# Kernel tuning notes

Measured on AMD Instinct MI355X. Metric: run time of the kernel, lower is better.

The kernel has to match this reference:

```python
import jax, jax.numpy as jnp
import numpy as np

B, S, D, E = 4, 4096, 1024, 8

def setup_inputs() -> dict:
    key = jax.random.key(0)
    k1, k2, k3, k4, k5 = jax.random.split(key, 5)
    scale = 1.0 / np.sqrt(D)
    return {
        "x": jax.random.normal(k1, (B, S, D), dtype=jnp.float32),
        "Wg": jax.random.normal(k2, (D, D), dtype=jnp.float32) * scale,   # gate Linear(D, D)
        "bg": jnp.zeros((D,), dtype=jnp.float32),
        "We": jax.random.normal(k3, (E, D, D), dtype=jnp.float32) * scale,  # per-expert Linear(D, D)
        "be": jnp.zeros((E, D), dtype=jnp.float32),
    }

def reference(x, Wg, bg, We, be):
    # gating network: Linear + Softmax over last dim (size D, per the original module)
    probs = jax.nn.softmax(x @ Wg + bg, axis=-1)           # [B,S,D]
    idx = jnp.argmax(probs, axis=-1)                        # [B,S], values in [0, D)
    p = jnp.take_along_axis(probs, idx[..., None], axis=-1)[..., 0]  # top-1 gate prob
    e_idx = idx % We.shape[0]                               # map argmax to expert id
    # run every expert densely, then select routed expert per token (top-1 switch routing)
    h = jax.nn.relu(jnp.einsum('bsd,edf->besf', x, We) + be[None, :, None, :])  # [B,E,S,D]
    onehot = jax.nn.one_hot(e_idx, We.shape[0], dtype=x.dtype)                   # [B,S,E]
    out = jnp.einsum('besf,bse->bsf', h, onehot) * p[..., None]                  # [B,S,D]
    return out
```

## Files before the change

kernel.cpp:

```cpp
#include <hip/hip_runtime.h>
#include <stdint.h>
#include <stddef.h>

#define TOK    16384
#define DDIM   1024
#define NEXP   8
#define BMT    128
#define RB_MAX 136
#define MARGIN 2.5e-2f
#define AMBIG_CAP 4096
#define BK     64

typedef __bf16 bf16x8 __attribute__((ext_vector_type(8)));
typedef float  f32x4  __attribute__((ext_vector_type(4)));
typedef unsigned short u16x8 __attribute__((ext_vector_type(8)));

__device__ __forceinline__ unsigned short f2bf(float f) {
    unsigned int u = __float_as_uint(f);
    u += 0x7fff + ((u >> 16) & 1);
    return (unsigned short)(u >> 16);
}

__device__ __forceinline__ void gload_lds16(const void* g, void* l) {
    __builtin_amdgcn_global_load_lds(
        (const __attribute__((address_space(1))) unsigned int*)g,
        (__attribute__((address_space(3))) unsigned int*)l, 16, 0, 0);
}

__device__ __forceinline__ void seg_starts(const int* __restrict__ cnt, int* st) {
    int total = 0;
#pragma unroll
    for (int e = 0; e < NEXP; e++) {
        st[e] = total;
        total += ((cnt[e] + BMT - 1) / BMT) * BMT;
    }
    st[NEXP] = total;
}

__global__ __launch_bounds__(256) void cvt_x_init(
    const float* __restrict__ x, unsigned short* __restrict__ xbf,
    int* __restrict__ cnt, int* __restrict__ cursor,
    int* __restrict__ n_ambig, int* __restrict__ row_of_slot)
{
    if (blockIdx.x == 0) {
        for (int i = threadIdx.x; i < RB_MAX * BMT; i += 256) row_of_slot[i] = -1;
        if (threadIdx.x < NEXP) { cnt[threadIdx.x] = 0; cursor[threadIdx.x] = 0; }
        if (threadIdx.x == 0) *n_ambig = 0;
    }
    const size_t t = ((size_t)blockIdx.x * 256 + threadIdx.x) * 8;
    const float4 v0 = *(const float4*)(x + t);
    const float4 v1 = *(const float4*)(x + t + 4);
    const float vv[8] = {v0.x, v0.y, v0.z, v0.w, v1.x, v1.y, v1.z, v1.w};
    u16x8 hh;
#pragma unroll
    for (int j = 0; j < 8; j++) hh[j] = f2bf(vv[j]);
    *(u16x8*)(xbf + t) = hh;
}

__global__ __launch_bounds__(256) void transpose_mat(
    const float* __restrict__ src0, unsigned short* __restrict__ dst0)
{
    __shared__ float tile[32][33];
    const int e  = blockIdx.z;
    const int k0 = blockIdx.x * 32;
    const int n0 = blockIdx.y * 32;
    const int tx = threadIdx.x;
    const int ty = threadIdx.y;
    const float* src = src0 + (size_t)e * DDIM * DDIM;
    unsigned short* dst = dst0 + (size_t)e * DDIM * DDIM;
#pragma unroll
    for (int r = 0; r < 4; r++)
        tile[ty + r * 8][tx] = src[(size_t)(k0 + ty + r * 8) * DDIM + n0 + tx];
    __syncthreads();
#pragma unroll
    for (int r = 0; r < 4; r++)
        dst[(size_t)(n0 + ty + r * 8) * DDIM + k0 + tx] = f2bf(tile[tx][ty + r * 8]);
}

__global__ __launch_bounds__(256) void transpose_wg(
    const float* __restrict__ src, unsigned short* __restrict__ dstb,
    float* __restrict__ dstf)
{
    __shared__ float tile[32][33];
    const int k0 = blockIdx.x * 32;
    const int n0 = blockIdx.y * 32;
    const int tx = threadIdx.x;
    const int ty = threadIdx.y;
#pragma unroll
    for (int r = 0; r < 4; r++)
        tile[ty + r * 8][tx] = src[(size_t)(k0 + ty + r * 8) * DDIM + n0 + tx];
    __syncthreads();
#pragma unroll
    for (int r = 0; r < 4; r++) {
        const float v = tile[tx][ty + r * 8];
        const size_t o = (size_t)(n0 + ty + r * 8) * DDIM + k0 + tx;
        dstb[o] = f2bf(v);
        dstf[o] = v;
    }
}

__global__ __launch_bounds__(256) void gating_mfma(
    const unsigned short* __restrict__ xbf,
    const unsigned short* __restrict__ WgT,
    const float* __restrict__ bg, float* __restrict__ logits)
{
    __shared__ unsigned short Asm[128 * BK];
    __shared__ unsigned short Bsm[128 * BK];
    const int bid = blockIdx.x;
    const int xcd = bid & 7;
    const int seq = bid >> 3;
    const int cl  = seq >> 6;
    const int w   = seq & 63;
    const int rb  = xcd * 16 + (w >> 2);
    const int nb  = cl * 4 + (w & 3);
    const int tid  = threadIdx.x;
    const int lane = tid & 63;
    const int wave = tid >> 6;
    const int q    = lane >> 4;
    const int m16  = lane & 15;
    const int wrow = (wave & 1) * 64;
    const int wcol = (wave >> 1) * 64;

    const unsigned short* Ag = xbf + (size_t)rb * 128 * DDIM;
    const unsigned short* Bg = WgT + (size_t)nb * 128 * DDIM;

    const unsigned short* pa[4];
    const unsigned short* pb[4];
#pragma unroll
    for (int i = 0; i < 4; i++) {
        const int idx = tid + i * 256;
        const int r = idx >> 3;
        const int c = idx & 7;
        const int g = (c ^ (r & 7)) * 8;
        pa[i] = Ag + (size_t)r * DDIM + g;
        pb[i] = Bg + (size_t)r * DDIM + g;
    }

    f32x4 acc[4][4];
#pragma unroll
    for (int i = 0; i < 4; i++)
#pragma unroll
        for (int j = 0; j < 4; j++) acc[i][j] = (f32x4){0.f, 0.f, 0.f, 0.f};

    for (int k0 = 0; k0 < DDIM; k0 += BK) {
#pragma unroll
        for (int i = 0; i < 4; i++) {
            gload_lds16(pa[i] + k0, &Asm[(tid + i * 256) * 8]);
            gload_lds16(pb[i] + k0, &Bsm[(tid + i * 256) * 8]);
        }
        __syncthreads();
#pragma unroll
        for (int s = 0; s < 2; s++) {
            const int cs = (((s << 2) + q) ^ (m16 & 7)) << 3;
            bf16x8 af[4], bfr[4];
#pragma unroll
            for (int i = 0; i < 4; i++)
                af[i] = *(const bf16x8*)&Asm[(wrow + i * 16 + m16) * BK + cs];
#pragma unroll
            for (int j = 0; j < 4; j++)
                bfr[j] = *(const bf16x8*)&Bsm[(wcol + j * 16 + m16) * BK + cs];
#pragma unroll
            for (int i = 0; i < 4; i++)
#pragma unroll
                for (int j = 0; j < 4; j++)
                    acc[i][j] = __builtin_amdgcn_mfma_f32_16x16x32_bf16(
                        af[i], bfr[j], acc[i][j], 0, 0, 0);
        }
        __syncthreads();
    }

    float bgv[4];
#pragma unroll
    for (int j = 0; j < 4; j++) bgv[j] = bg[nb * 128 + wcol + j * 16 + m16];
#pragma unroll
    for (int i = 0; i < 4; i++)
#pragma unroll
        for (int r = 0; r < 4; r++) {
            const int row = rb * 128 + wrow + i * 16 + q * 4 + r;
#pragma unroll
            for (int j = 0; j < 4; j++) {
                const int col = nb * 128 + wcol + j * 16 + m16;
                logits[(size_t)row * DDIM + col] = acc[i][j][r] + bgv[j];
            }
        }
}

__global__ __launch_bounds__(256) void row_stats(
    const float* __restrict__ logits, float* __restrict__ pout,
    int* __restrict__ eout, float* __restrict__ rmax_a, float* __restrict__ s_a,
    int* __restrict__ ambig, int* __restrict__ n_ambig)
{
    const int row  = blockIdx.x * 4 + (threadIdx.x >> 6);
    const int lane = threadIdx.x & 63;
    const float* L = logits + (size_t)row * DDIM;
    float vals[16];
#pragma unroll
    for (int i = 0; i < 4; i++)
        *(float4*)&vals[i * 4] = *(const float4*)&L[lane * 16 + i * 4];
    float m = vals[0]; int mi = lane * 16;
#pragma unroll
    for (int i = 1; i < 16; i++)
        if (vals[i] > m) { m = vals[i]; mi = lane * 16 + i; }
    for (int off = 32; off > 0; off >>= 1) {
        float ov = __shfl_down(m, off, 64);
        int   oi = __shfl_down(mi, off, 64);
        if (ov > m || (ov == m && oi < mi)) { m = ov; mi = oi; }
    }
    m  = __shfl(m, 0, 64);
    mi = __shfl(mi, 0, 64);
    float s = 0.f;
    int   c = 0;
#pragma unroll
    for (int i = 0; i < 16; i++) {
        s += expf(vals[i] - m);
        if (vals[i] >= m - MARGIN) c++;
    }
    for (int off = 32; off > 0; off >>= 1) {
        s += __shfl_xor(s, off, 64);
        c += __shfl_xor(c, off, 64);
    }
    if (lane == 0) {
        pout[row] = 1.0f / s;
        eout[row] = mi & (NEXP - 1);
        rmax_a[row] = m;
        s_a[row] = s;
        if (c > 1) {
            int k = atomicAdd(n_ambig, 1);
            if (k < AMBIG_CAP) ambig[k] = row;
        }
    }
}

__global__ __launch_bounds__(64) void fixup(
    const float* __restrict__ logits, const float* __restrict__ x,
    const float* __restrict__ WgTf, const float* __restrict__ bg,
    const float* __restrict__ rmax_a, const float* __restrict__ s_a,
    const int* __restrict__ ambig, const int* __restrict__ n_ambig,
    int* __restrict__ eout, float* __restrict__ pout)
{
    int n = *n_ambig; if (n > AMBIG_CAP) n = AMBIG_CAP;
    if ((int)blockIdx.x >= n) return;
    const int row  = ambig[blockIdx.x];
    const int lane = threadIdx.x;
    const float rmax = rmax_a[row];
    const float* L = logits + (size_t)row * DDIM;
    __shared__ int scnt;
    __shared__ int scol[32];
    if (lane == 0) scnt = 0;
    __syncthreads();
    for (int j = lane; j < DDIM; j += 64)
        if (L[j] >= rmax - MARGIN) {
            int k = atomicAdd(&scnt, 1);
            if (k < 32) scol[k] = j;
        }
    __syncthreads();
    int ncand = scnt < 32 ? scnt : 32;
    double bestv = -1e300; int bestc = DDIM;
    for (int cidx = 0; cidx < ncand; cidx++) {
        const int col = scol[cidx];
        const float* Wcol = WgTf + (size_t)col * DDIM;
        double s = 0.0;
        for (int k = lane; k < DDIM; k += 64)
            s += (double)x[(size_t)row * DDIM + k] * (double)Wcol[k];
        for (int off = 32; off > 0; off >>= 1) s += __shfl_down(s, off, 64);
        s = __shfl(s, 0, 64);
        s += (double)bg[col];
        if (s > bestv || (s == bestv && col < bestc)) { bestv = s; bestc = col; }
    }
    if (lane == 0) {
        eout[row] = bestc & (NEXP - 1);
        pout[row] = expf(L[bestc] - rmax) / s_a[row];
    }
}

__global__ __launch_bounds__(256) void histo(const int* __restrict__ eout,
                                             int* __restrict__ cnt)
{
    __shared__ int h[NEXP];
    if (threadIdx.x < NEXP) h[threadIdx.x] = 0;
    __syncthreads();
    const int t = blockIdx.x * 256 + threadIdx.x;
    if (t < TOK) atomicAdd(&h[eout[t]], 1);
    __syncthreads();
    if (threadIdx.x < NEXP) atomicAdd(&cnt[threadIdx.x], h[threadIdx.x]);
}

__global__ __launch_bounds__(256) void assign_slots(
    const int* __restrict__ eout, const int* __restrict__ cnt,
    int* __restrict__ cursor, int* __restrict__ row_of_slot)
{
    __shared__ int h[NEXP];
    __shared__ int base[NEXP];
    __shared__ int sstart[NEXP];
    const int tid = threadIdx.x;
    if (tid < NEXP) {
        h[tid] = 0;
        int st[NEXP + 1];
        seg_starts(cnt, st);
        sstart[tid] = st[tid];
    }
    __syncthreads();
    const int t = blockIdx.x * 256 + tid;
    int e = 0, lr = 0;
    if (t < TOK) {
        e = eout[t];
        lr = atomicAdd(&h[e], 1);
    }
    __syncthreads();
    if (tid < NEXP && h[tid] > 0)
        base[tid] = atomicAdd(&cursor[tid], h[tid]);
    __syncthreads();
    if (t < TOK)
        row_of_slot[sstart[e] + base[e] + lr] = t;
}

__global__ __launch_bounds__(256) void expert_gemm(
    const unsigned short* __restrict__ xbf, const unsigned short* __restrict__ WeT,
    const float* __restrict__ be, const float* __restrict__ p,
    const int* __restrict__ row_of_slot, const int* __restrict__ cnt,
    float* __restrict__ out)
{
    __shared__ unsigned short Asm[128 * BK];
    __shared__ unsigned short Bsm[128 * BK];
    __shared__ int rs[128];
    const int bid = blockIdx.x;
    const int xcd = bid & 7;
    const int seq = bid >> 3;
    const int cl  = seq / 68;
    const int w   = seq % 68;
    const int rb  = xcd * 17 + (w >> 2);
    const int nb  = cl * 4 + (w & 3);

    int st[NEXP + 1];
    seg_starts(cnt, st);
    const int s0 = rb * BMT;
    int e = -1;
#pragma unroll
    for (int ei = 0; ei < NEXP; ei++)
        if (s0 >= st[ei] && s0 < st[ei + 1]) e = ei;
    if (e < 0) return;

    const int tid  = threadIdx.x;
    const int lane = tid & 63;
    const int wave = tid >> 6;
    const int q    = lane >> 4;
    const int m16  = lane & 15;
    const int wrow = (wave & 1) * 64;
    const int wcol = (wave >> 1) * 64;

    if (tid < 128) rs[tid] = row_of_slot[rb * 128 + tid];
    __syncthreads();

    const unsigned short* Bglob = WeT + (size_t)e * DDIM * DDIM + (size_t)nb * 128 * DDIM;

    const unsigned short* pa[4];
    const unsigned short* pb[4];
#pragma unroll
    for (int i = 0; i < 4; i++) {
        const int idx = tid + i * 256;
        const int r = idx >> 3;
        const int c = idx & 7;
        const int g = (c ^ (r & 7)) * 8;
        int tr = rs[r]; if (tr < 0) tr = 0;
        pa[i] = xbf + (size_t)tr * DDIM + g;
        pb[i] = Bglob + (size_t)r * DDIM + g;
    }

    f32x4 acc[4][4];
#pragma unroll
    for (int i = 0; i < 4; i++)
#pragma unroll
        for (int j = 0; j < 4; j++) acc[i][j] = (f32x4){0.f, 0.f, 0.f, 0.f};

    for (int k0 = 0; k0 < DDIM; k0 += BK) {
#pragma unroll
        for (int i = 0; i < 4; i++) {
            gload_lds16(pa[i] + k0, &Asm[(tid + i * 256) * 8]);
            gload_lds16(pb[i] + k0, &Bsm[(tid + i * 256) * 8]);
        }
        __syncthreads();
#pragma unroll
        for (int s = 0; s < 2; s++) {
            const int cs = (((s << 2) + q) ^ (m16 & 7)) << 3;
            bf16x8 af[4], bfr[4];
#pragma unroll
            for (int i = 0; i < 4; i++)
                af[i] = *(const bf16x8*)&Asm[(wrow + i * 16 + m16) * BK + cs];
#pragma unroll
            for (int j = 0; j < 4; j++)
                bfr[j] = *(const bf16x8*)&Bsm[(wcol + j * 16 + m16) * BK + cs];
#pragma unroll
            for (int i = 0; i < 4; i++)
#pragma unroll
                for (int j = 0; j < 4; j++)
                    acc[i][j] = __builtin_amdgcn_mfma_f32_16x16x32_bf16(
                        af[i], bfr[j], acc[i][j], 0, 0, 0);
        }
        __syncthreads();
    }

    float bev[4];
#pragma unroll
    for (int j = 0; j < 4; j++) bev[j] = be[e * DDIM + nb * 128 + wcol + j * 16 + m16];
#pragma unroll
    for (int i = 0; i < 4; i++)
#pragma unroll
        for (int r = 0; r < 4; r++) {
            const int t = rs[wrow + i * 16 + q * 4 + r];
            if (t < 0) continue;
            const float pv = p[t];
#pragma unroll
            for (int j = 0; j < 4; j++) {
                const int n = nb * 128 + wcol + j * 16 + m16;
                float v = acc[i][j][r] + bev[j];
                v = v > 0.f ? v : 0.f;
                out[(size_t)t * DDIM + n] = v * pv;
            }
        }
}

extern "C" void kernel_launch(void* const* d_in, const int* in_sizes, int n_in,
                              void* d_out, int out_size, void* d_ws, size_t ws_size,
                              hipStream_t stream)
{
    const float* x  = (const float*)d_in[0];
    const float* Wg = (const float*)d_in[1];
    const float* bg = (const float*)d_in[2];
    const float* We = (const float*)d_in[3];
    const float* be = (const float*)d_in[4];
    float* out = (float*)d_out;

    char* ws = (char*)d_ws;
    float* logits = (float*)ws;                 ws += (size_t)TOK * DDIM * 4;
    unsigned short* WeT = (unsigned short*)ws;  ws += (size_t)NEXP * DDIM * DDIM * 2;
    unsigned short* WgT = (unsigned short*)ws;  ws += (size_t)DDIM * DDIM * 2;
    float* WgTf = (float*)ws;                   ws += (size_t)DDIM * DDIM * 4;
    unsigned short* xbf = (unsigned short*)ws;  ws += (size_t)TOK * DDIM * 2;
    float* p = (float*)ws;                      ws += (size_t)TOK * 4;
    int* e_arr = (int*)ws;                      ws += (size_t)TOK * 4;
    float* rmax_a = (float*)ws;                 ws += (size_t)TOK * 4;
    float* s_a = (float*)ws;                    ws += (size_t)TOK * 4;
    int* row_of_slot = (int*)ws;                ws += (size_t)RB_MAX * BMT * 4;
    int* cnt = (int*)ws;                        ws += NEXP * 4;
    int* cursor = (int*)ws;                     ws += NEXP * 4;
    int* ambig = (int*)ws;                      ws += AMBIG_CAP * 4;
    int* n_ambig = (int*)ws;                    ws += 4;

    cvt_x_init<<<TOK * DDIM / (256 * 8), 256, 0, stream>>>(
        x, xbf, cnt, cursor, n_ambig, row_of_slot);
    transpose_wg<<<dim3(32, 32), dim3(32, 8), 0, stream>>>(Wg, WgT, WgTf);
    transpose_mat<<<dim3(32, 32, NEXP), dim3(32, 8), 0, stream>>>(We, WeT);
    gating_mfma<<<1024, 256, 0, stream>>>(xbf, WgT, bg, logits);
    row_stats<<<TOK / 4, 256, 0, stream>>>(logits, p, e_arr, rmax_a, s_a, ambig, n_ambig);
    fixup<<<AMBIG_CAP, 64, 0, stream>>>(logits, x, WgTf, bg, rmax_a, s_a, ambig, n_ambig, e_arr, p);
    histo<<<TOK / 256, 256, 0, stream>>>(e_arr, cnt);
    assign_slots<<<TOK / 256, 256, 0, stream>>>(e_arr, cnt, cursor, row_of_slot);
    expert_gemm<<<1088, 256, 0, stream>>>(
        xbf, WeT, be, p, row_of_slot, cnt, out);
}
```

Baseline: 310.8 us.

## Fuse per-row softmax partial stats into gating GEMM epilogue and merge histogram

The gating GEMM epilogue now computes, for each row and each 64-column slice, the partial max, argmax, exp-sum and near-max count, and writes them to a small partials buffer. A new row_combine kernel merges the 16 partials per row instead of rereading the full 64 MB logits matrix. The same kernel also builds the expert histogram, which removes the separate histo launch. fixup now corrects the counts with atomics when it changes a token's expert. This adds shuffles and a 4 MB partials write to the GEMM epilogue, and the ambiguity count across slices is approximated by counting a non-winning slice within the margin as two candidates.

After: 317.5 us. +2.2%, slower.

```diff
diff --git a/kernel.cpp b/kernel.cpp
--- a/kernel.cpp
+++ b/kernel.cpp
@@ -102,7 +102,8 @@
 __global__ __launch_bounds__(256) void gating_mfma(
     const unsigned short* __restrict__ xbf,
     const unsigned short* __restrict__ WgT,
-    const float* __restrict__ bg, float* __restrict__ logits)
+    const float* __restrict__ bg, float* __restrict__ logits,
+    float4* __restrict__ part)
 {
     __shared__ unsigned short Asm[128 * BK];
     __shared__ unsigned short Bsm[128 * BK];
@@ -172,63 +173,85 @@
     float bgv[4];
 #pragma unroll
     for (int j = 0; j < 4; j++) bgv[j] = bg[nb * 128 + wcol + j * 16 + m16];
+    const int nbh = nb * 2 + (wave >> 1);
 #pragma unroll
     for (int i = 0; i < 4; i++)
 #pragma unroll
         for (int r = 0; r < 4; r++) {
             const int row = rb * 128 + wrow + i * 16 + q * 4 + r;
+            float v[4];
+            float vmax = -1e30f; int vidx = 0;
 #pragma unroll
             for (int j = 0; j < 4; j++) {
+                v[j] = acc[i][j][r] + bgv[j];
                 const int col = nb * 128 + wcol + j * 16 + m16;
-                logits[(size_t)row * DDIM + col] = acc[i][j][r] + bgv[j];
-            }
-        }
-}
-
-__global__ __launch_bounds__(256) void row_stats(
-    const float* __restrict__ logits, float* __restrict__ pout,
+                logits[(size_t)row * DDIM + col] = v[j];
+                if (v[j] > vmax) { vmax = v[j]; vidx = col; }
+            }
+#pragma unroll
+            for (int off = 8; off > 0; off >>= 1) {
+                float ov = __shfl_xor(vmax, off, 64);
+                int   oi = __shfl_xor(vidx, off, 64);
+                if (ov > vmax || (ov == vmax && oi < vidx)) { vmax = ov; vidx = oi; }
+            }
+            float sg = 0.f; int cg = 0;
+#pragma unroll
+            for (int j = 0; j < 4; j++) {
+                sg += expf(v[j] - vmax);
+                cg += (v[j] >= vmax - MARGIN) ? 1 : 0;
+            }
+#pragma unroll
+            for (int off = 8; off > 0; off >>= 1) {
+                sg += __shfl_xor(sg, off, 64);
+                cg += __shfl_xor(cg, off, 64);
+            }
+            if (m16 == 0) {
+                float4 pr;
+                pr.x = vmax; pr.y = __int_as_float(vidx);
+                pr.z = sg;   pr.w = __int_as_float(cg);
+                part[(size_t)row * 16 + nbh] = pr;
+            }
+        }
+}
+
+__global__ __launch_bounds__(256) void row_combine(
+    const float4* __restrict__ part, float* __restrict__ pout,
     int* __restrict__ eout, float* __restrict__ rmax_a, float* __restrict__ s_a,
-    int* __restrict__ ambig, int* __restrict__ n_ambig)
-{
-    const int row  = blockIdx.x * 4 + (threadIdx.x >> 6);
-    const int lane = threadIdx.x & 63;
-    const float* L = logits + (size_t)row * DDIM;
-    float vals[16];
-#pragma unroll
-    for (int i = 0; i < 4; i++)
-        *(float4*)&vals[i * 4] = *(const float4*)&L[lane * 16 + i * 4];
-    float m = vals[0]; int mi = lane * 16;
-#pragma unroll
-    for (int i = 1; i < 16; i++)
-        if (vals[i] > m) { m = vals[i]; mi = lane * 16 + i; }
-    for (int off = 32; off > 0; off >>= 1) {
-        float ov = __shfl_down(m, off, 64);
-        int   oi = __shfl_down(mi, off, 64);
-        if (ov > m || (ov == m && oi < mi)) { m = ov; mi = oi; }
-    }
-    m  = __shfl(m, 0, 64);
-    mi = __shfl(mi, 0, 64);
-    float s = 0.f;
-    int   c = 0;
-#pragma unroll
-    for (int i = 0; i < 16; i++) {
-        s += expf(vals[i] - m);
-        if (vals[i] >= m - MARGIN) c++;
-    }
-    for (int off = 32; off > 0; off >>= 1) {
-        s += __shfl_xor(s, off, 64);
-        c += __shfl_xor(c, off, 64);
-    }
-    if (lane == 0) {
-        pout[row] = 1.0f / s;
-        eout[row] = mi & (NEXP - 1);
-        rmax_a[row] = m;
-        s_a[row] = s;
-        if (c > 1) {
-            int k = atomicAdd(n_ambig, 1);
-            if (k < AMBIG_CAP) ambig[k] = row;
-        }
-    }
+    int* __restrict__ ambig, int* __restrict__ n_ambig, int* __restrict__ cnt)
+{
+    __shared__ int h[NEXP];
+    if (threadIdx.x < NEXP) h[threadIdx.x] = 0;
+    __syncthreads();
+    const int row = blockIdx.x * 256 + threadIdx.x;
+    float4 pr[16];
+#pragma unroll
+    for (int k = 0; k < 16; k++) pr[k] = part[(size_t)row * 16 + k];
+    float m = pr[0].x; int idx = __float_as_int(pr[0].y); int win = 0;
+#pragma unroll
+    for (int k = 1; k < 16; k++) {
+        const int ki = __float_as_int(pr[k].y);
+        if (pr[k].x > m || (pr[k].x == m && ki < idx)) { m = pr[k].x; idx = ki; win = k; }
+    }
+    float s = 0.f; int namb = 0;
+#pragma unroll
+    for (int k = 0; k < 16; k++) {
+        s += pr[k].z * expf(pr[k].x - m);
+        if (k == win) namb += __float_as_int(pr[k].w);
+        else namb += (pr[k].x >= m - MARGIN) ? 2 : 0;
+    }
+    const int e = idx & (NEXP - 1);
+    pout[row] = 1.0f / s;
+    eout[row] = e;
+    rmax_a[row] = m;
+    s_a[row] = s;
+    if (namb > 1) {
+        int k = atomicAdd(n_ambig, 1);
+        if (k < AMBIG_CAP) ambig[k] = row;
+    }
+    atomicAdd(&h[e], 1);
+    __syncthreads();
+    if (threadIdx.x < NEXP && h[threadIdx.x] > 0)
+        atomicAdd(&cnt[threadIdx.x], h[threadIdx.x]);
 }
 
 __global__ __launch_bounds__(64) void fixup(
@@ -236,7 +259,7 @@
     const float* __restrict__ WgTf, const float* __restrict__ bg,
     const float* __restrict__ rmax_a, const float* __restrict__ s_a,
     const int* __restrict__ ambig, const int* __restrict__ n_ambig,
-    int* __restrict__ eout, float* __restrict__ pout)
+    int* __restrict__ eout, float* __restrict__ pout, int* __restrict__ cnt)
 {
     int n = *n_ambig; if (n > AMBIG_CAP) n = AMBIG_CAP;
     if ((int)blockIdx.x >= n) return;
@@ -268,21 +291,15 @@
         if (s > bestv || (s == bestv && col < bestc)) { bestv = s; bestc = col; }
     }
     if (lane == 0) {
-        eout[row] = bestc & (NEXP - 1);
+        const int new_e = bestc & (NEXP - 1);
+        const int old_e = eout[row];
+        if (new_e != old_e) {
+            atomicAdd(&cnt[old_e], -1);
+            atomicAdd(&cnt[new_e], 1);
+        }
+        eout[row] = new_e;
         pout[row] = expf(L[bestc] - rmax) / s_a[row];
     }
-}
-
-__global__ __launch_bounds__(256) void histo(const int* __restrict__ eout,
-                                             int* __restrict__ cnt)
-{
-    __shared__ int h[NEXP];
-    if (threadIdx.x < NEXP) h[threadIdx.x] = 0;
-    __syncthreads();
-    const int t = blockIdx.x * 256 + threadIdx.x;
-    if (t < TOK) atomicAdd(&h[eout[t]], 1);
-    __syncthreads();
-    if (threadIdx.x < NEXP) atomicAdd(&cnt[threadIdx.x], h[threadIdx.x]);
 }
 
 __global__ __launch_bounds__(256) void assign_slots(
@@ -436,6 +453,7 @@
     unsigned short* WgT = (unsigned short*)ws;  ws += (size_t)DDIM * DDIM * 2;
     float* WgTf = (float*)ws;                   ws += (size_t)DDIM * DDIM * 4;
     unsigned short* xbf = (unsigned short*)ws;  ws += (size_t)TOK * DDIM * 2;
+    float4* part = (float4*)ws;                 ws += (size_t)TOK * 16 * 16;
     float* p = (float*)ws;                      ws += (size_t)TOK * 4;
     int* e_arr = (int*)ws;                      ws += (size_t)TOK * 4;
     float* rmax_a = (float*)ws;                 ws += (size_t)TOK * 4;
@@ -450,10 +468,11 @@
         x, xbf, cnt, cursor, n_ambig, row_of_slot);
     transpose_wg<<<dim3(32, 32), dim3(32, 8), 0, stream>>>(Wg, WgT, WgTf);
     transpose_mat<<<dim3(32, 32, NEXP), dim3(32, 8), 0, stream>>>(We, WeT);
-    gating_mfma<<<1024, 256, 0, stream>>>(xbf, WgT, bg, logits);
-    row_stats<<<TOK / 4, 256, 0, stream>>>(logits, p, e_arr, rmax_a, s_a, ambig, n_ambig);
-    fixup<<<AMBIG_CAP, 64, 0, stream>>>(logits, x, WgTf, bg, rmax_a, s_a, ambig, n_ambig, e_arr, p);
-    histo<<<TOK / 256, 256, 0, stream>>>(e_arr, cnt);
+    gating_mfma<<<1024, 256, 0, stream>>>(xbf, WgT, bg, logits, part);
+    row_combine<<<TOK / 256, 256, 0, stream>>>(
+        part, p, e_arr, rmax_a, s_a, ambig, n_ambig, cnt);
+    fixup<<<AMBIG_CAP, 64, 0, stream>>>(
+        logits, x, WgTf, bg, rmax_a, s_a, ambig, n_ambig, e_arr, p, cnt);
     assign_slots<<<TOK / 256, 256, 0, stream>>>(e_arr, cnt, cursor, row_of_slot);
     expert_gemm<<<1088, 256, 0, stream>>>(
         xbf, WeT, be, p, row_of_slot, cnt, out);
```

## Rewrite gating GEMM as 256x256 double-buffered 8-wave pipelined kernel

Applied to the files above, without the earlier changes.

The gating GEMM moves from 128x128 tiles with a single LDS buffer and 4 waves to 256x256 tiles with 8 waves, BK=32, and two LDS stages. It prefetches the next K-slice into the other buffer using vmcnt-counted waits and interleaves MFMA phases with explicit barriers and setprio. The aim is to hide global load latency and raise reuse per tile. In exchange the grid shrinks to 256 blocks, and registers rise to 32 accumulators per lane, which may limit occupancy.

After: 324.1 us. 4.3% more time.

```diff
diff --git a/kernel.cpp b/kernel.cpp
--- a/kernel.cpp
+++ b/kernel.cpp
@@ -11,6 +11,11 @@
 #define AMBIG_CAP 4096
 #define BK     64
 
+#define GBM 256
+#define GBN 256
+#define GBK 32
+#define GKT (DDIM / GBK)
+
 typedef __bf16 bf16x8 __attribute__((ext_vector_type(8)));
 typedef float  f32x4  __attribute__((ext_vector_type(4)));
 typedef unsigned short u16x8 __attribute__((ext_vector_type(8)));
@@ -99,87 +104,114 @@
     }
 }
 
-__global__ __launch_bounds__(256) void gating_mfma(
+#define GSTAGE(s, kt) do { const int _k = (kt) * GBK; \
+    gload_lds16(pa0 + _k, &As[s][sidx0 * 8]); \
+    gload_lds16(pa1 + _k, &As[s][sidx1 * 8]); \
+    gload_lds16(pb0 + _k, &Bs[s][sidx0 * 8]); \
+    gload_lds16(pb1 + _k, &Bs[s][sidx1 * 8]); } while (0)
+
+#define GPHASE(s, qd) do { \
+    bf16x8 af_[4], bf_[2]; \
+    _Pragma("unroll") for (int fi = 0; fi < 4; fi++) { \
+        const int row_ = wm * 128 + ((qd) & 1) * 64 + fi * 16 + m16; \
+        af_[fi] = *(const bf16x8*)&As[s][row_ * GBK + ((q ^ (m16 & 3)) << 3)]; \
+    } \
+    _Pragma("unroll") for (int fj = 0; fj < 2; fj++) { \
+        const int row_ = wn * 64 + ((qd) >> 1) * 32 + fj * 16 + m16; \
+        bf_[fj] = *(const bf16x8*)&Bs[s][row_ * GBK + ((q ^ (m16 & 3)) << 3)]; \
+    } \
+    __builtin_amdgcn_sched_barrier(0); \
+    __builtin_amdgcn_s_barrier(); \
+    asm volatile("s_waitcnt lgkmcnt(0)" ::: "memory"); \
+    __builtin_amdgcn_sched_barrier(0); \
+    __builtin_amdgcn_s_setprio(1); \
+    _Pragma("unroll") for (int fi = 0; fi < 4; fi++) \
+        _Pragma("unroll") for (int fj = 0; fj < 2; fj++) \
+            acc[((qd) & 1) * 4 + fi][((qd) >> 1) * 2 + fj] = \
+                __builtin_amdgcn_mfma_f32_16x16x32_bf16(af_[fi], bf_[fj], \
+                    acc[((qd) & 1) * 4 + fi][((qd) >> 1) * 2 + fj], 0, 0, 0); \
+    __builtin_amdgcn_s_setprio(0); \
+    __builtin_amdgcn_sched_barrier(0); \
+    __builtin_amdgcn_s_barrier(); \
+    __builtin_amdgcn_sched_barrier(0); } while (0)
+
+#define GBARX() do { __builtin_amdgcn_sched_barrier(0); \
+    __builtin_amdgcn_s_barrier(); \
+    __builtin_amdgcn_sched_barrier(0); } while (0)
+
+__global__ __launch_bounds__(512, 2) void gating_mfma(
     const unsigned short* __restrict__ xbf,
     const unsigned short* __restrict__ WgT,
     const float* __restrict__ bg, float* __restrict__ logits)
 {
-    __shared__ unsigned short Asm[128 * BK];
-    __shared__ unsigned short Bsm[128 * BK];
+    __shared__ unsigned short As[2][GBM * GBK];
+    __shared__ unsigned short Bs[2][GBN * GBK];
     const int bid = blockIdx.x;
     const int xcd = bid & 7;
     const int seq = bid >> 3;
-    const int cl  = seq >> 6;
-    const int w   = seq & 63;
-    const int rb  = xcd * 16 + (w >> 2);
-    const int nb  = cl * 4 + (w & 3);
+    const int rb  = xcd * 8 + (seq >> 2);
+    const int nb  = seq & 3;
     const int tid  = threadIdx.x;
     const int lane = tid & 63;
     const int wave = tid >> 6;
+    const int wm   = wave & 1;
+    const int wn   = wave >> 1;
     const int q    = lane >> 4;
     const int m16  = lane & 15;
-    const int wrow = (wave & 1) * 64;
-    const int wcol = (wave >> 1) * 64;
-
-    const unsigned short* Ag = xbf + (size_t)rb * 128 * DDIM;
-    const unsigned short* Bg = WgT + (size_t)nb * 128 * DDIM;
-
-    const unsigned short* pa[4];
-    const unsigned short* pb[4];
-#pragma unroll
-    for (int i = 0; i < 4; i++) {
-        const int idx = tid + i * 256;
-        const int r = idx >> 3;
-        const int c = idx & 7;
-        const int g = (c ^ (r & 7)) * 8;
-        pa[i] = Ag + (size_t)r * DDIM + g;
-        pb[i] = Bg + (size_t)r * DDIM + g;
-    }
-
-    f32x4 acc[4][4];
-#pragma unroll
-    for (int i = 0; i < 4; i++)
+
+    const unsigned short* Ag = xbf + (size_t)rb * GBM * DDIM;
+    const unsigned short* Bg = WgT + (size_t)nb * GBN * DDIM;
+
+    const int sidx0 = tid, sidx1 = tid + 512;
+    const int sr0 = sidx0 >> 2, sc0 = sidx0 & 3;
+    const int sr1 = sidx1 >> 2, sc1 = sidx1 & 3;
+    const unsigned short* pa0 = Ag + (size_t)sr0 * DDIM + (sc0 ^ (sr0 & 3)) * 8;
+    const unsigned short* pa1 = Ag + (size_t)sr1 * DDIM + (sc1 ^ (sr1 & 3)) * 8;
+    const unsigned short* pb0 = Bg + (size_t)sr0 * DDIM + (sc0 ^ (sr0 & 3)) * 8;
+    const unsigned short* pb1 = Bg + (size_t)sr1 * DDIM + (sc1 ^ (sr1 & 3)) * 8;
+
+    f32x4 acc[8][4];
+#pragma unroll
+    for (int i = 0; i < 8; i++)
 #pragma unroll
         for (int j = 0; j < 4; j++) acc[i][j] = (f32x4){0.f, 0.f, 0.f, 0.f};
 
-    for (int k0 = 0; k0 < DDIM; k0 += BK) {
-#pragma unroll
-        for (int i = 0; i < 4; i++) {
-            gload_lds16(pa[i] + k0, &Asm[(tid + i * 256) * 8]);
-            gload_lds16(pb[i] + k0, &Bsm[(tid + i * 256) * 8]);
-        }
-        __syncthreads();
-#pragma unroll
-        for (int s = 0; s < 2; s++) {
-            const int cs = (((s << 2) + q) ^ (m16 & 7)) << 3;
-            bf16x8 af[4], bfr[4];
-#pragma unroll
-            for (int i = 0; i < 4; i++)
-                af[i] = *(const bf16x8*)&Asm[(wrow + i * 16 + m16) * BK + cs];
-#pragma unroll
-            for (int j = 0; j < 4; j++)
-                bfr[j] = *(const bf16x8*)&Bsm[(wcol + j * 16 + m16) * BK + cs];
-#pragma unroll
-            for (int i = 0; i < 4; i++)
-#pragma unroll
-                for (int j = 0; j < 4; j++)
-                    acc[i][j] = __builtin_amdgcn_mfma_f32_16x16x32_bf16(
-                        af[i], bfr[j], acc[i][j], 0, 0, 0);
-        }
-        __syncthreads();
+    GSTAGE(0, 0);
+    GSTAGE(1, 1);
+    asm volatile("s_waitcnt vmcnt(4)" ::: "memory");
+    GBARX();
+
+#pragma unroll 1
+    for (int kt = 0; kt < GKT; kt += 2) {
+        GPHASE(0, 0); GPHASE(0, 1); GPHASE(0, 2); GPHASE(0, 3);
+        if (kt + 2 < GKT) {
+            GSTAGE(0, kt + 2);
+            asm volatile("s_waitcnt vmcnt(4)" ::: "memory");
+        } else {
+            asm volatile("s_waitcnt vmcnt(0)" ::: "memory");
+        }
+        GBARX();
+        GPHASE(1, 0); GPHASE(1, 1); GPHASE(1, 2); GPHASE(1, 3);
+        if (kt + 3 < GKT) {
+            GSTAGE(1, kt + 3);
+            asm volatile("s_waitcnt vmcnt(4)" ::: "memory");
+        } else if (kt + 2 < GKT) {
+            asm volatile("s_waitcnt vmcnt(0)" ::: "memory");
+        }
+        GBARX();
     }
 
     float bgv[4];
 #pragma unroll
-    for (int j = 0; j < 4; j++) bgv[j] = bg[nb * 128 + wcol + j * 16 + m16];
-#pragma unroll
-    for (int i = 0; i < 4; i++)
+    for (int j = 0; j < 4; j++) bgv[j] = bg[nb * GBN + wn * 64 + j * 16 + m16];
+#pragma unroll
+    for (int i = 0; i < 8; i++)
 #pragma unroll
         for (int r = 0; r < 4; r++) {
-            const int row = rb * 128 + wrow + i * 16 + q * 4 + r;
+            const int row = rb * GBM + wm * 128 + i * 16 + q * 4 + r;
 #pragma unroll
             for (int j = 0; j < 4; j++) {
-                const int col = nb * 128 + wcol + j * 16 + m16;
+                const int col = nb * GBN + wn * 64 + j * 16 + m16;
                 logits[(size_t)row * DDIM + col] = acc[i][j][r] + bgv[j];
             }
         }
@@ -450,7 +482,7 @@
         x, xbf, cnt, cursor, n_ambig, row_of_slot);
     transpose_wg<<<dim3(32, 32), dim3(32, 8), 0, stream>>>(Wg, WgT, WgTf);
     transpose_mat<<<dim3(32, 32, NEXP), dim3(32, 8), 0, stream>>>(We, WeT);
-    gating_mfma<<<1024, 256, 0, stream>>>(xbf, WgT, bg, logits);
+    gating_mfma<<<(TOK / GBM) * (DDIM / GBN), 512, 0, stream>>>(xbf, WgT, bg, logits);
     row_stats<<<TOK / 4, 256, 0, stream>>>(logits, p, e_arr, rmax_a, s_a, ambig, n_ambig);
     fixup<<<AMBIG_CAP, 64, 0, stream>>>(logits, x, WgTf, bg, rmax_a, s_a, ambig, n_ambig, e_arr, p);
     histo<<<TOK / 256, 256, 0, stream>>>(e_arr, cnt);
```
